# Kernel tuning notes

Hardware: AMD Instinct MI355X
Metric: run time of the kernel (lower is better)

## Reference

```python
import jax, jax.numpy as jnp
import numpy as np

DIM = 1024
N_HEADS = 16


def setup_inputs() -> dict:
    key = jax.random.key(0)
    ks = jax.random.split(key, 7)
    x = jax.random.normal(ks[0], (2, 2048, DIM), dtype=jnp.float32)
    wq = jax.random.normal(ks[1], (DIM, DIM), dtype=jnp.float32) * 0.01
    wk = jax.random.normal(ks[2], (DIM, DIM), dtype=jnp.float32) * 0.01
    wv = jax.random.normal(ks[3], (DIM, DIM), dtype=jnp.float32) * 0.01
    wo = jax.random.normal(ks[4], (DIM, DIM), dtype=jnp.float32) * 0.01
    w1 = jax.random.normal(ks[5], (DIM, 4 * DIM), dtype=jnp.float32) * 0.01
    w2 = jax.random.normal(ks[6], (4 * DIM, DIM), dtype=jnp.float32) * 0.01
    return {"x": x, "wq": wq, "wk": wk, "wv": wv, "wo": wo, "w1": w1, "w2": w2}


def reference(x, wq, wk, wv, wo, w1, w2):
    bsz, seqlen, dim = x.shape
    head_dim = dim // N_HEADS
    # project and split heads: [b, h, s, d]
    q = (x @ wq).reshape(bsz, seqlen, N_HEADS, head_dim).transpose(0, 2, 1, 3)
    k = (x @ wk).reshape(bsz, seqlen, N_HEADS, head_dim).transpose(0, 2, 1, 3)
    v = (x @ wv).reshape(bsz, seqlen, N_HEADS, head_dim).transpose(0, 2, 1, 3)
    scale = head_dim ** (-0.5)
    # full [b, h, s, s] score matrix, as in the original module
    attn = jnp.einsum('bhqd,bhkd->bhqk', q, k) * scale
    attn = jax.nn.softmax(attn, axis=-1)
    out = jnp.einsum('bhqk,bhkd->bhqd', attn, v)
    out = out.transpose(0, 2, 1, 3).reshape(bsz, seqlen, dim)
    x = x + out @ wo
    h = jax.nn.relu(x @ w1)
    x = x + h @ w2
    return x
```

## Files before the change

kernel.cpp:

```cpp
#include <hip/hip_runtime.h>
#include <hip/hip_bf16.h>
#include <stdint.h>

typedef __attribute__((ext_vector_type(8))) short short8_t;
typedef __attribute__((ext_vector_type(4))) short short4_t;
typedef __attribute__((ext_vector_type(4))) float floatx4;

#define MTOT 4096
#define DIMV 1024
#define SEQ  2048
#define NH   16
#define HD   64
#define QKV_LD 3072
#define KVB 64
#define NKT (SEQ / KVB)

__device__ __forceinline__ floatx4 mfma16(short8_t a, short8_t b, floatx4 c) {
    return __builtin_amdgcn_mfma_f32_16x16x32_bf16(a, b, c, 0, 0, 0);
}

__device__ __forceinline__ void gload_lds16(const void* g, void* l) {
    __builtin_amdgcn_global_load_lds(
        (const __attribute__((address_space(1))) void*)g,
        (__attribute__((address_space(3))) void*)l,
        16, 0, 0);
}

__device__ __forceinline__ short bf16bits(float f) {
    return __builtin_bit_cast(short, __float2bfloat16(f));
}

__device__ __forceinline__ short8_t frag64(const __hip_bfloat16* base, int row, int col0) {
    int off = row * 64 + (((col0 >> 3) ^ (row & 7)) << 3);
    return *(const short8_t*)(base + off);
}

struct bf4 { __hip_bfloat16 a, b, c, d; };

__global__ void prep_all(const float* __restrict__ x,
                         const float* __restrict__ wq, const float* __restrict__ wk,
                         const float* __restrict__ wv, const float* __restrict__ wo,
                         const float* __restrict__ w1, const float* __restrict__ w2,
                         __hip_bfloat16* __restrict__ xb,
                         __hip_bfloat16* __restrict__ wqkvt, __hip_bfloat16* __restrict__ wot,
                         __hip_bfloat16* __restrict__ w1t, __hip_bfloat16* __restrict__ w2t) {
    __shared__ float tile[32][33];
    int bid = blockIdx.x;
    int t = threadIdx.x;
    if (bid >= 12288) {
        int i = (bid - 12288) * 256 + t;
        const float4* xv = reinterpret_cast<const float4*>(x) + i;
        float4 v = *xv;
        bf4 r;
        r.a = __float2bfloat16(v.x); r.b = __float2bfloat16(v.y);
        r.c = __float2bfloat16(v.z); r.d = __float2bfloat16(v.w);
        *reinterpret_cast<bf4*>(xb + (size_t)i * 4) = r;
        return;
    }
    const float* w; __hip_bfloat16* wt; int K, N, K32, tau; float scale = 1.0f;
    if (bid < 1024)      { w = wq; wt = wqkvt;                 K = 1024; N = 1024; K32 = 32;  tau = bid;        scale = 0.125f; }
    else if (bid < 2048) { w = wk; wt = wqkvt + 1024 * 1024;   K = 1024; N = 1024; K32 = 32;  tau = bid - 1024; }
    else if (bid < 3072) { w = wv; wt = wqkvt + 2048 * 1024;   K = 1024; N = 1024; K32 = 32;  tau = bid - 2048; }
    else if (bid < 4096) { w = wo; wt = wot;                   K = 1024; N = 1024; K32 = 32;  tau = bid - 3072; }
    else if (bid < 8192) { w = w1; wt = w1t;                   K = 1024; N = 4096; K32 = 32;  tau = bid - 4096; }
    else                 { w = w2; wt = w2t;                   K = 4096; N = 1024; K32 = 128; tau = bid - 8192; }
    int k0 = (tau % K32) * 32, n0 = (tau / K32) * 32;
    int tx = t & 31, ty = t >> 5;
    #pragma unroll
    for (int r = 0; r < 32; r += 8)
        tile[ty + r][tx] = w[(size_t)(k0 + ty + r) * N + n0 + tx];
    __syncthreads();
    #pragma unroll
    for (int r = 0; r < 32; r += 8)
        wt[(size_t)(n0 + ty + r) * K + k0 + tx] = __float2bfloat16(tile[tx][ty + r] * scale);
}

__global__ void vtrans(const __hip_bfloat16* __restrict__ v, int ld,
                       __hip_bfloat16* __restrict__ vt) {
    __shared__ __hip_bfloat16 tile[32][33];
    int s0 = blockIdx.x * 32;
    int c0 = blockIdx.y * 32;
    int tx = threadIdx.x & 31, ty = threadIdx.x >> 5;
    #pragma unroll
    for (int r = 0; r < 32; r += 8)
        tile[ty + r][tx] = v[(size_t)(s0 + ty + r) * ld + c0 + tx];
    __syncthreads();
    int b = s0 >> 11;
    int h = c0 >> 6;
    int d0 = c0 & 63;
    #pragma unroll
    for (int r = 0; r < 32; r += 8)
        vt[(size_t)((b * NH + h) * HD + d0 + ty + r) * SEQ + (s0 & 2047) + tx] = tile[tx][ty + r];
}

__global__ void combine2(const float* __restrict__ p0, const float* __restrict__ p1,
                         const float* __restrict__ resid, float* __restrict__ out, int n4) {
    int i = blockIdx.x * 256 + threadIdx.x;
    if (i < n4) {
        float4 a = reinterpret_cast<const float4*>(p0)[i];
        float4 b = reinterpret_cast<const float4*>(p1)[i];
        float4 c = reinterpret_cast<const float4*>(resid)[i];
        float4 r;
        r.x = a.x + b.x + c.x; r.y = a.y + b.y + c.y;
        r.z = a.z + b.z + c.z; r.w = a.w + b.w + c.w;
        reinterpret_cast<float4*>(out)[i] = r;
    }
}

template <int EPI>
__launch_bounds__(256)
__global__ void gemm_bt(const __hip_bfloat16* __restrict__ A,
                        const __hip_bfloat16* __restrict__ Bt,
                        int M, int N, int K, int lda, int ldb, float scale,
                        const float* __restrict__ resid,
                        float* __restrict__ outf,
                        __hip_bfloat16* __restrict__ outb, size_t zout) {
    __shared__ __align__(16) __hip_bfloat16 As[2][128 * 32];
    __shared__ __align__(16) __hip_bfloat16 Bs[2][128 * 32];
    A += (size_t)blockIdx.z * K;
    Bt += (size_t)blockIdx.z * K;
    outf += (size_t)blockIdx.z * zout;
    const int t = threadIdx.x;
    const int l = t & 63;
    const int w = t >> 6;
    const int wr = w >> 1, wc = w & 1;
    const int lrow = l & 15;
    const int lk = (l >> 4) << 3;
    const int li4 = (l >> 4) << 2;
    const int arow0 = blockIdx.x * 128;
    const int brow0 = blockIdx.y * 128;

    floatx4 acc[4][4];
    #pragma unroll
    for (int m = 0; m < 4; m++)
        #pragma unroll
        for (int n = 0; n < 4; n++)
            acc[m][n] = (floatx4){0.f, 0.f, 0.f, 0.f};

    const int nkt = K >> 5;
    const int sr = t >> 2, sc8 = (t & 3) << 3;
    const __hip_bfloat16* ga0 = A + (size_t)(arow0 + sr) * lda + sc8;
    const __hip_bfloat16* gb0 = Bt + (size_t)(brow0 + sr) * ldb + sc8;

    gload_lds16(ga0,                    (char*)As[0] + t * 16);
    gload_lds16(ga0 + (size_t)64 * lda, (char*)As[0] + 4096 + t * 16);
    gload_lds16(gb0,                    (char*)Bs[0] + t * 16);
    gload_lds16(gb0 + (size_t)64 * ldb, (char*)Bs[0] + 4096 + t * 16);
    asm volatile("s_waitcnt vmcnt(0)" ::: "memory");
    __builtin_amdgcn_s_barrier();
    __builtin_amdgcn_sched_barrier(0);

    int cur = 0;
    for (int kt = 0; kt < nkt; ++kt) {
        if (kt + 1 < nkt) {
            const __hip_bfloat16* ga = ga0 + (kt + 1) * 32;
            const __hip_bfloat16* gb = gb0 + (kt + 1) * 32;
            gload_lds16(ga,                    (char*)As[cur ^ 1] + t * 16);
            gload_lds16(ga + (size_t)64 * lda, (char*)As[cur ^ 1] + 4096 + t * 16);
            gload_lds16(gb,                    (char*)Bs[cur ^ 1] + t * 16);
            gload_lds16(gb + (size_t)64 * ldb, (char*)Bs[cur ^ 1] + 4096 + t * 16);
        }
        short8_t af[4], bfr[4];
        #pragma unroll
        for (int m = 0; m < 4; m++)
            af[m] = *(const short8_t*)((const char*)As[cur] + (((wr << 6) + (m << 4) + lrow) << 6) + (lk << 1));
        #pragma unroll
        for (int n = 0; n < 4; n++)
            bfr[n] = *(const short8_t*)((const char*)Bs[cur] + (((wc << 6) + (n << 4) + lrow) << 6) + (lk << 1));
        #pragma unroll
        for (int m = 0; m < 4; m++)
            #pragma unroll
            for (int n = 0; n < 4; n++)
                acc[m][n] = mfma16(af[m], bfr[n], acc[m][n]);
        asm volatile("s_waitcnt vmcnt(0)" ::: "memory");
        __builtin_amdgcn_s_barrier();
        __builtin_amdgcn_sched_barrier(0);
        cur ^= 1;
    }

    #pragma unroll
    for (int m = 0; m < 4; m++) {
        #pragma unroll
        for (int n = 0; n < 4; n++) {
            int row = arow0 + (wr << 6) + (m << 4) + li4;
            int col = brow0 + (wc << 6) + (n << 4) + lrow;
            #pragma unroll
            for (int i = 0; i < 4; i++) {
                float vv = acc[m][n][i] * scale;
                size_t off = (size_t)(row + i) * N + col;
                if (EPI == 0) {
                    outb[off] = __float2bfloat16(vv);
                } else if (EPI == 1) {
                    outb[off] = __float2bfloat16(vv > 0.f ? vv : 0.f);
                } else if (EPI == 2) {
                    float f = vv + resid[off];
                    outf[off] = f;
                    outb[off] = __float2bfloat16(f);
                } else if (EPI == 3) {
                    outf[off] = vv + resid[off];
                } else {
                    outf[off] = vv;
                }
            }
        }
    }
}

__launch_bounds__(256, 3)
__global__ void attn_kernel(const __hip_bfloat16* __restrict__ qkv,
                            const __hip_bfloat16* __restrict__ vt,
                            __hip_bfloat16* __restrict__ o) {
    __shared__ __align__(16) __hip_bfloat16 Ks[2][KVB * 64];
    __shared__ __align__(16) __hip_bfloat16 Vs[2][KVB * 64];
    __shared__ __align__(16) __hip_bfloat16 Ps[128 * 64];
    const int t = threadIdx.x, l = t & 63, w = t >> 6;
    const int bh = blockIdx.y;
    const int b = bh >> 4, h = bh & 15;
    const int q0 = blockIdx.x * 128;
    const int lq = l & 15;
    const int lg = l >> 4;

    const __hip_bfloat16* qbase = qkv + (size_t)(b * SEQ + q0) * QKV_LD + h * HD;
    const __hip_bfloat16* kbase = qkv + (size_t)(b * SEQ) * QKV_LD + 1024 + h * HD;
    const __hip_bfloat16* vbase = vt + (size_t)(bh * HD) * SEQ;

    #pragma unroll
    for (int s = 0; s < 4; ++s) {
        int u = t + 256 * s;
        int r = u >> 3, c = (u & 7) ^ (r & 7);
        gload_lds16(qbase + (size_t)r * QKV_LD + c * 8, (char*)Ps + u * 16);
    }
    #pragma unroll
    for (int s = 0; s < 2; ++s) {
        int u = t + 256 * s;
        int r = u >> 3, c = (u & 7) ^ (r & 7);
        gload_lds16(kbase + (size_t)r * QKV_LD + c * 8, (char*)Ks[0] + u * 16);
        gload_lds16(vbase + (size_t)r * SEQ + c * 8,    (char*)Vs[0] + u * 16);
    }
    asm volatile("s_waitcnt vmcnt(0)" ::: "memory");
    __builtin_amdgcn_s_barrier();
    __builtin_amdgcn_sched_barrier(0);

    short8_t qf[2][2];
    #pragma unroll
    for (int m = 0; m < 2; m++)
        #pragma unroll
        for (int kc = 0; kc < 2; kc++)
            qf[m][kc] = frag64(Ps, (w << 5) + (m << 4) + lq, kc * 32 + lg * 8);
    asm volatile("s_waitcnt lgkmcnt(0)" ::: "memory");
    __builtin_amdgcn_s_barrier();
    __builtin_amdgcn_sched_barrier(0);

    float l_part[2] = {0.f, 0.f};
    floatx4 o_acc[2][4];
    #pragma unroll
    for (int m = 0; m < 2; m++)
        #pragma unroll
        for (int n = 0; n < 4; n++)
            o_acc[m][n] = (floatx4){0.f, 0.f, 0.f, 0.f};

    int cur = 0;
    for (int kt = 0; kt < NKT; ++kt) {
        if (kt + 1 < NKT) {
            int kv = (kt + 1) * KVB;
            #pragma unroll
            for (int s = 0; s < 2; ++s) {
                int u = t + 256 * s;
                int r = u >> 3, c = (u & 7) ^ (r & 7);
                gload_lds16(kbase + (size_t)(kv + r) * QKV_LD + c * 8,
                            (char*)Ks[cur ^ 1] + u * 16);
                gload_lds16(vbase + (size_t)r * SEQ + kv + c * 8,
                            (char*)Vs[cur ^ 1] + u * 16);
            }
        }

        const __hip_bfloat16* kc_base = Ks[cur];
        floatx4 sa[2][4];
        #pragma unroll
        for (int m = 0; m < 2; m++)
            #pragma unroll
            for (int n = 0; n < 4; n++)
                sa[m][n] = (floatx4){0.f, 0.f, 0.f, 0.f};
        #pragma unroll
        for (int n = 0; n < 4; n++) {
            #pragma unroll
            for (int kc = 0; kc < 2; kc++) {
                short8_t kf = frag64(kc_base, n * 16 + lq, kc * 32 + lg * 8);
                sa[0][n] = mfma16(kf, qf[0][kc], sa[0][n]);
                sa[1][n] = mfma16(kf, qf[1][kc], sa[1][n]);
            }
        }

        short4_t pk[2][4];
        #pragma unroll
        for (int m = 0; m < 2; m++) {
            #pragma unroll
            for (int n = 0; n < 4; n++) {
                float p0 = __expf(sa[m][n][0]);
                float p1 = __expf(sa[m][n][1]);
                float p2 = __expf(sa[m][n][2]);
                float p3 = __expf(sa[m][n][3]);
                l_part[m] += (p0 + p1) + (p2 + p3);
                short4_t pv;
                pv[0] = bf16bits(p0);
                pv[1] = bf16bits(p1);
                pv[2] = bf16bits(p2);
                pv[3] = bf16bits(p3);
                pk[m][n] = pv;
            }
        }

        #pragma unroll
        for (int m = 0; m < 2; m++) {
            int row = (w << 5) + (m << 4) + lq;
            #pragma unroll
            for (int n = 0; n < 4; n++) {
                int k0 = n * 16 + lg * 4;
                char* dst = (char*)Ps + row * 128 +
                            ((((k0 >> 3) ^ (row & 7)) << 4) | ((k0 & 4) << 1));
                *(short4_t*)dst = pk[m][n];
            }
        }
        asm volatile("s_waitcnt lgkmcnt(0)" ::: "memory");
        __builtin_amdgcn_s_barrier();
        __builtin_amdgcn_sched_barrier(0);

        const __hip_bfloat16* vc_base = Vs[cur];
        #pragma unroll
        for (int kc = 0; kc < 2; kc++) {
            short8_t pf0 = frag64(Ps, (w << 5) + lq,      kc * 32 + lg * 8);
            short8_t pf1 = frag64(Ps, (w << 5) + 16 + lq, kc * 32 + lg * 8);
            #pragma unroll
            for (int n = 0; n < 4; n++) {
                short8_t vf = frag64(vc_base, n * 16 + lq, kc * 32 + lg * 8);
                o_acc[0][n] = mfma16(pf0, vf, o_acc[0][n]);
                o_acc[1][n] = mfma16(pf1, vf, o_acc[1][n]);
            }
        }
        asm volatile("s_waitcnt vmcnt(0)" ::: "memory");
        __builtin_amdgcn_s_barrier();
        __builtin_amdgcn_sched_barrier(0);
        cur ^= 1;
    }

    __hip_bfloat16* obase = o + (size_t)(b * SEQ + q0) * DIMV + h * HD;
    #pragma unroll
    for (int m = 0; m < 2; m++) {
        float lr = l_part[m];
        lr += __shfl_xor(lr, 16, 64);
        lr += __shfl_xor(lr, 32, 64);
        #pragma unroll
        for (int i = 0; i < 4; i++) {
            float li = 1.0f / __shfl(lr, (lg << 2) + i, 16);
            int row = (w << 5) + (m << 4) + (lg << 2) + i;
            #pragma unroll
            for (int n = 0; n < 4; n++) {
                obase[(size_t)row * DIMV + n * 16 + lq] =
                    __float2bfloat16(o_acc[m][n][i] * li);
            }
        }
    }
}

extern "C" void kernel_launch(void* const* d_in, const int* in_sizes, int n_in,
                              void* d_out, int out_size, void* d_ws, size_t ws_size,
                              hipStream_t stream) {
    const float* x  = (const float*)d_in[0];
    const float* wq = (const float*)d_in[1];
    const float* wk = (const float*)d_in[2];
    const float* wv = (const float*)d_in[3];
    const float* wo = (const float*)d_in[4];
    const float* w1 = (const float*)d_in[5];
    const float* w2 = (const float*)d_in[6];
    float* outf = (float*)d_out;

    char* ws = (char*)d_ws;
    const size_t MB = (size_t)1 << 20;
    __hip_bfloat16* xb    = (__hip_bfloat16*)(ws + 0 * MB);
    __hip_bfloat16* wqkvt = (__hip_bfloat16*)(ws + 8 * MB);
    __hip_bfloat16* wot   = (__hip_bfloat16*)(ws + 14 * MB);
    __hip_bfloat16* w1t   = (__hip_bfloat16*)(ws + 16 * MB);
    __hip_bfloat16* w2t   = (__hip_bfloat16*)(ws + 24 * MB);
    __hip_bfloat16* qkvb  = (__hip_bfloat16*)(ws + 32 * MB);
    __hip_bfloat16* vtp   = (__hip_bfloat16*)(ws + 56 * MB);
    __hip_bfloat16* atb   = (__hip_bfloat16*)(ws + 64 * MB);
    __hip_bfloat16* x1b   = (__hip_bfloat16*)(ws + 72 * MB);
    __hip_bfloat16* hb    = (__hip_bfloat16*)(ws + 80 * MB);
    float* part0 = (float*)(ws + 32 * MB);

    prep_all<<<dim3(16384), dim3(256), 0, stream>>>(x, wq, wk, wv, wo, w1, w2,
                                                    xb, wqkvt, wot, w1t, w2t);

    gemm_bt<0><<<dim3(32, 24), dim3(256), 0, stream>>>(xb, wqkvt, MTOT, QKV_LD, 1024,
                                                       1024, 1024, 1.0f, nullptr, nullptr, qkvb, 0);
    vtrans<<<dim3(128, 32), dim3(256), 0, stream>>>(qkvb + 2048, QKV_LD, vtp);

    attn_kernel<<<dim3(16, 32), dim3(256), 0, stream>>>(qkvb, vtp, atb);

    gemm_bt<2><<<dim3(32, 8), dim3(256), 0, stream>>>(atb, wot, MTOT, 1024, 1024,
                                                      1024, 1024, 1.0f, x, outf, x1b, 0);
    gemm_bt<1><<<dim3(32, 32), dim3(256), 0, stream>>>(x1b, w1t, MTOT, 4096, 1024,
                                                       1024, 1024, 1.0f, nullptr, nullptr, hb, 0);
    gemm_bt<4><<<dim3(32, 8, 2), dim3(256), 0, stream>>>(hb, w2t, MTOT, 1024, 2048,
                                                         4096, 4096, 1.0f, nullptr, part0, nullptr,
                                                         (size_t)MTOT * 1024);
    combine2<<<dim3(4096), dim3(256), 0, stream>>>(part0, part0 + (size_t)MTOT * 1024,
                                                   outf, outf, MTOT * 1024 / 4);
}
```

Baseline: 333.3 us.

## Triple-buffer GEMM loads and halve attention query tile per block

The GEMM mainloop moves from double to triple buffering, prefetching two k-tiles ahead and waiting with vmcnt(4) so global loads overlap more compute. The attention kernel now processes 64 query rows per block (16 per wave) instead of 128. This doubles the grid, raises the occupancy hint to 4, and drops the barrier between the P writes and the P reads because each wave only touches its own rows. The costs are more LDS in the GEMM and twice as many K/V tile loads per head in attention.

```diff
diff --git a/kernel.cpp b/kernel.cpp
--- a/kernel.cpp
+++ b/kernel.cpp
@@ -115,8 +115,8 @@
                         const float* __restrict__ resid,
                         float* __restrict__ outf,
                         __hip_bfloat16* __restrict__ outb, size_t zout) {
-    __shared__ __align__(16) __hip_bfloat16 As[2][128 * 32];
-    __shared__ __align__(16) __hip_bfloat16 Bs[2][128 * 32];
+    __shared__ __align__(16) __hip_bfloat16 As[3][128 * 32];
+    __shared__ __align__(16) __hip_bfloat16 Bs[3][128 * 32];
     A += (size_t)blockIdx.z * K;
     Bt += (size_t)blockIdx.z * K;
     outf += (size_t)blockIdx.z * zout;
@@ -142,24 +142,24 @@
     const __hip_bfloat16* ga0 = A + (size_t)(arow0 + sr) * lda + sc8;
     const __hip_bfloat16* gb0 = Bt + (size_t)(brow0 + sr) * ldb + sc8;
 
-    gload_lds16(ga0,                    (char*)As[0] + t * 16);
-    gload_lds16(ga0 + (size_t)64 * lda, (char*)As[0] + 4096 + t * 16);
-    gload_lds16(gb0,                    (char*)Bs[0] + t * 16);
-    gload_lds16(gb0 + (size_t)64 * ldb, (char*)Bs[0] + 4096 + t * 16);
-    asm volatile("s_waitcnt vmcnt(0)" ::: "memory");
+#define GSTAGE(KT, BUF) do { \
+        const __hip_bfloat16* ga_ = ga0 + (KT) * 32; \
+        const __hip_bfloat16* gb_ = gb0 + (KT) * 32; \
+        gload_lds16(ga_,                    (char*)As[BUF] + t * 16); \
+        gload_lds16(ga_ + (size_t)64 * lda, (char*)As[BUF] + 4096 + t * 16); \
+        gload_lds16(gb_,                    (char*)Bs[BUF] + t * 16); \
+        gload_lds16(gb_ + (size_t)64 * ldb, (char*)Bs[BUF] + 4096 + t * 16); \
+    } while (0)
+
+    GSTAGE(0, 0);
+    GSTAGE(1, 1);
+    asm volatile("s_waitcnt vmcnt(4)" ::: "memory");
     __builtin_amdgcn_s_barrier();
     __builtin_amdgcn_sched_barrier(0);
 
-    int cur = 0;
     for (int kt = 0; kt < nkt; ++kt) {
-        if (kt + 1 < nkt) {
-            const __hip_bfloat16* ga = ga0 + (kt + 1) * 32;
-            const __hip_bfloat16* gb = gb0 + (kt + 1) * 32;
-            gload_lds16(ga,                    (char*)As[cur ^ 1] + t * 16);
-            gload_lds16(ga + (size_t)64 * lda, (char*)As[cur ^ 1] + 4096 + t * 16);
-            gload_lds16(gb,                    (char*)Bs[cur ^ 1] + t * 16);
-            gload_lds16(gb + (size_t)64 * ldb, (char*)Bs[cur ^ 1] + 4096 + t * 16);
-        }
+        const int cur = kt % 3;
+        if (kt + 2 < nkt) GSTAGE(kt + 2, (kt + 2) % 3);
         short8_t af[4], bfr[4];
         #pragma unroll
         for (int m = 0; m < 4; m++)
@@ -172,11 +172,12 @@
             #pragma unroll
             for (int n = 0; n < 4; n++)
                 acc[m][n] = mfma16(af[m], bfr[n], acc[m][n]);
-        asm volatile("s_waitcnt vmcnt(0)" ::: "memory");
+        if (kt + 2 < nkt) asm volatile("s_waitcnt vmcnt(4)" ::: "memory");
+        else              asm volatile("s_waitcnt vmcnt(0)" ::: "memory");
         __builtin_amdgcn_s_barrier();
         __builtin_amdgcn_sched_barrier(0);
-        cur ^= 1;
-    }
+    }
+#undef GSTAGE
 
     #pragma unroll
     for (int m = 0; m < 4; m++) {
@@ -206,17 +207,17 @@
     }
 }
 
-__launch_bounds__(256, 3)
+__launch_bounds__(256, 4)
 __global__ void attn_kernel(const __hip_bfloat16* __restrict__ qkv,
                             const __hip_bfloat16* __restrict__ vt,
                             __hip_bfloat16* __restrict__ o) {
     __shared__ __align__(16) __hip_bfloat16 Ks[2][KVB * 64];
     __shared__ __align__(16) __hip_bfloat16 Vs[2][KVB * 64];
-    __shared__ __align__(16) __hip_bfloat16 Ps[128 * 64];
+    __shared__ __align__(16) __hip_bfloat16 Ps[64 * 64];
     const int t = threadIdx.x, l = t & 63, w = t >> 6;
     const int bh = blockIdx.y;
     const int b = bh >> 4, h = bh & 15;
-    const int q0 = blockIdx.x * 128;
+    const int q0 = blockIdx.x * 64;
     const int lq = l & 15;
     const int lg = l >> 4;
 
@@ -225,15 +226,10 @@
     const __hip_bfloat16* vbase = vt + (size_t)(bh * HD) * SEQ;
 
     #pragma unroll
-    for (int s = 0; s < 4; ++s) {
+    for (int s = 0; s < 2; ++s) {
         int u = t + 256 * s;
         int r = u >> 3, c = (u & 7) ^ (r & 7);
         gload_lds16(qbase + (size_t)r * QKV_LD + c * 8, (char*)Ps + u * 16);
-    }
-    #pragma unroll
-    for (int s = 0; s < 2; ++s) {
-        int u = t + 256 * s;
-        int r = u >> 3, c = (u & 7) ^ (r & 7);
         gload_lds16(kbase + (size_t)r * QKV_LD + c * 8, (char*)Ks[0] + u * 16);
         gload_lds16(vbase + (size_t)r * SEQ + c * 8,    (char*)Vs[0] + u * 16);
     }
@@ -241,23 +237,19 @@
     __builtin_amdgcn_s_barrier();
     __builtin_amdgcn_sched_barrier(0);
 
-    short8_t qf[2][2];
-    #pragma unroll
-    for (int m = 0; m < 2; m++)
-        #pragma unroll
-        for (int kc = 0; kc < 2; kc++)
-            qf[m][kc] = frag64(Ps, (w << 5) + (m << 4) + lq, kc * 32 + lg * 8);
+    short8_t qf[2];
+    #pragma unroll
+    for (int kc = 0; kc < 2; kc++)
+        qf[kc] = frag64(Ps, (w << 4) + lq, kc * 32 + lg * 8);
     asm volatile("s_waitcnt lgkmcnt(0)" ::: "memory");
     __builtin_amdgcn_s_barrier();
     __builtin_amdgcn_sched_barrier(0);
 
-    float l_part[2] = {0.f, 0.f};
-    floatx4 o_acc[2][4];
-    #pragma unroll
-    for (int m = 0; m < 2; m++)
-        #pragma unroll
-        for (int n = 0; n < 4; n++)
-            o_acc[m][n] = (floatx4){0.f, 0.f, 0.f, 0.f};
+    float l_part = 0.f;
+    floatx4 o_acc[4];
+    #pragma unroll
+    for (int n = 0; n < 4; n++)
+        o_acc[n] = (floatx4){0.f, 0.f, 0.f, 0.f};
 
     int cur = 0;
     for (int kt = 0; kt < NKT; ++kt) {
@@ -274,67 +266,59 @@
             }
         }
 
-        const __hip_bfloat16* kc_base = Ks[cur];
-        floatx4 sa[2][4];
-        #pragma unroll
-        for (int m = 0; m < 2; m++)
-            #pragma unroll
-            for (int n = 0; n < 4; n++)
-                sa[m][n] = (floatx4){0.f, 0.f, 0.f, 0.f};
+        const __hip_bfloat16* kcb = Ks[cur];
+        floatx4 sa[4];
+        #pragma unroll
+        for (int n = 0; n < 4; n++)
+            sa[n] = (floatx4){0.f, 0.f, 0.f, 0.f};
         #pragma unroll
         for (int n = 0; n < 4; n++) {
             #pragma unroll
             for (int kc = 0; kc < 2; kc++) {
-                short8_t kf = frag64(kc_base, n * 16 + lq, kc * 32 + lg * 8);
-                sa[0][n] = mfma16(kf, qf[0][kc], sa[0][n]);
-                sa[1][n] = mfma16(kf, qf[1][kc], sa[1][n]);
-            }
-        }
-
-        short4_t pk[2][4];
-        #pragma unroll
-        for (int m = 0; m < 2; m++) {
-            #pragma unroll
-            for (int n = 0; n < 4; n++) {
-                float p0 = __expf(sa[m][n][0]);
-                float p1 = __expf(sa[m][n][1]);
-                float p2 = __expf(sa[m][n][2]);
-                float p3 = __expf(sa[m][n][3]);
-                l_part[m] += (p0 + p1) + (p2 + p3);
-                short4_t pv;
-                pv[0] = bf16bits(p0);
-                pv[1] = bf16bits(p1);
-                pv[2] = bf16bits(p2);
-                pv[3] = bf16bits(p3);
-                pk[m][n] = pv;
-            }
-        }
-
-        #pragma unroll
-        for (int m = 0; m < 2; m++) {
-            int row = (w << 5) + (m << 4) + lq;
+                short8_t kf = frag64(kcb, n * 16 + lq, kc * 32 + lg * 8);
+                sa[n] = mfma16(kf, qf[kc], sa[n]);
+            }
+        }
+
+        short4_t pk[4];
+        #pragma unroll
+        for (int n = 0; n < 4; n++) {
+            float p0 = __expf(sa[n][0]);
+            float p1 = __expf(sa[n][1]);
+            float p2 = __expf(sa[n][2]);
+            float p3 = __expf(sa[n][3]);
+            l_part += (p0 + p1) + (p2 + p3);
+            short4_t pv;
+            pv[0] = bf16bits(p0);
+            pv[1] = bf16bits(p1);
+            pv[2] = bf16bits(p2);
+            pv[3] = bf16bits(p3);
+            pk[n] = pv;
+        }
+
+        {
+            int row = (w << 4) + lq;
+            int rowb = row * 128;
+            int rw = row & 7;
             #pragma unroll
             for (int n = 0; n < 4; n++) {
                 int k0 = n * 16 + lg * 4;
-                char* dst = (char*)Ps + row * 128 +
-                            ((((k0 >> 3) ^ (row & 7)) << 4) | ((k0 & 4) << 1));
-                *(short4_t*)dst = pk[m][n];
+                char* dst = (char*)Ps + rowb +
+                            ((((k0 >> 3) ^ rw) << 4) | ((k0 & 4) << 1));
+                *(short4_t*)dst = pk[n];
             }
         }
         asm volatile("s_waitcnt lgkmcnt(0)" ::: "memory");
-        __builtin_amdgcn_s_barrier();
         __builtin_amdgcn_sched_barrier(0);
 
-        const __hip_bfloat16* vc_base = Vs[cur];
+        const __hip_bfloat16* vcb = Vs[cur];
         #pragma unroll
         for (int kc = 0; kc < 2; kc++) {
-            short8_t pf0 = frag64(Ps, (w << 5) + lq,      kc * 32 + lg * 8);
-            short8_t pf1 = frag64(Ps, (w << 5) + 16 + lq, kc * 32 + lg * 8);
+            short8_t pf = frag64(Ps, (w << 4) + lq, kc * 32 + lg * 8);
             #pragma unroll
             for (int n = 0; n < 4; n++) {
-                short8_t vf = frag64(vc_base, n * 16 + lq, kc * 32 + lg * 8);
-                o_acc[0][n] = mfma16(pf0, vf, o_acc[0][n]);
-                o_acc[1][n] = mfma16(pf1, vf, o_acc[1][n]);
+                short8_t vf = frag64(vcb, n * 16 + lq, kc * 32 + lg * 8);
+                o_acc[n] = mfma16(pf, vf, o_acc[n]);
             }
         }
         asm volatile("s_waitcnt vmcnt(0)" ::: "memory");
@@ -344,20 +328,17 @@
     }
 
     __hip_bfloat16* obase = o + (size_t)(b * SEQ + q0) * DIMV + h * HD;
-    #pragma unroll
-    for (int m = 0; m < 2; m++) {
-        float lr = l_part[m];
-        lr += __shfl_xor(lr, 16, 64);
-        lr += __shfl_xor(lr, 32, 64);
-        #pragma unroll
-        for (int i = 0; i < 4; i++) {
-            float li = 1.0f / __shfl(lr, (lg << 2) + i, 16);
-            int row = (w << 5) + (m << 4) + (lg << 2) + i;
-            #pragma unroll
-            for (int n = 0; n < 4; n++) {
-                obase[(size_t)row * DIMV + n * 16 + lq] =
-                    __float2bfloat16(o_acc[m][n][i] * li);
-            }
+    float lr = l_part;
+    lr += __shfl_xor(lr, 16, 64);
+    lr += __shfl_xor(lr, 32, 64);
+    #pragma unroll
+    for (int i = 0; i < 4; i++) {
+        float li = 1.0f / __shfl(lr, (lg << 2) + i, 16);
+        int row = (w << 4) + (lg << 2) + i;
+        #pragma unroll
+        for (int n = 0; n < 4; n++) {
+            obase[(size_t)row * DIMV + n * 16 + lq] =
+                __float2bfloat16(o_acc[n][i] * li);
         }
     }
 }
@@ -395,7 +376,7 @@
                                                        1024, 1024, 1.0f, nullptr, nullptr, qkvb, 0);
     vtrans<<<dim3(128, 32), dim3(256), 0, stream>>>(qkvb + 2048, QKV_LD, vtp);
 
-    attn_kernel<<<dim3(16, 32), dim3(256), 0, stream>>>(qkvb, vtp, atb);
+    attn_kernel<<<dim3(32, 32), dim3(256), 0, stream>>>(qkvb, vtp, atb);
 
     gemm_bt<2><<<dim3(32, 8), dim3(256), 0, stream>>>(atb, wot, MTOT, 1024, 1024,
                                                       1024, 1024, 1.0f, x, outf, x1b, 0);
```

Result: slower. 340.9 us (+2.3%).
